# Optimization experiments

Measured on AMD Instinct MI355X. Metric: run time of the kernel, lower is better.

The kernel has to match this reference:

```python
import jax, jax.numpy as jnp
import numpy as np

NUM_CLASSES = 172
IGNORE_INDEX = 255
DICE_WEIGHT = 0.5
EPS = 1e-7


def setup_inputs() -> dict:
    key = jax.random.key(0)
    k1, k2 = jax.random.split(key)
    pred = jax.random.normal(k1, (4, NUM_CLASSES, 256, 256), dtype=jnp.float32)
    target = jax.random.randint(k2, (4, 256, 256), 0, NUM_CLASSES, dtype=jnp.int32)
    return {"pred": pred, "target": target}


def reference(pred, target):
    # pred: [B, C, H, W] logits; target: [B, H, W] int labels (255 = ignore)
    C = NUM_CLASSES
    logp = jax.nn.log_softmax(pred, axis=1)  # [B, C, H, W]

    # ---- cross entropy with ignore_index (mean over valid pixels) ----
    valid = target != IGNORE_INDEX  # [B, H, W]
    safe_tgt = jnp.where(valid, target, 0)
    nll = -jnp.take_along_axis(logp, safe_tgt[:, None].astype(jnp.int32), axis=1)[:, 0]  # [B, H, W]
    n_valid = jnp.sum(valid)
    ce = jnp.sum(jnp.where(valid, nll, 0.0)) / jnp.maximum(n_valid, 1).astype(pred.dtype)

    # ---- dice loss: vectorized over classes (replaces per-class python loop) ----
    p = jnp.exp(logp)  # softmax probs [B, C, H, W]
    # intersection[c] = sum over pixels with target==c of p[:, c] at those pixels
    gathered = jnp.take_along_axis(p, safe_tgt[:, None].astype(jnp.int32), axis=1)[:, 0]  # [B, H, W]
    seg_ids = target.ravel().astype(jnp.int32)  # ignore pixels land in bucket 255, discarded
    inter = jax.ops.segment_sum(gathered.ravel(), seg_ids, num_segments=256)[:C]  # [C]
    counts = jax.ops.segment_sum(jnp.ones_like(gathered.ravel()), seg_ids, num_segments=256)[:C]
    union = jnp.sum(p, axis=(0, 2, 3)) + counts  # [C]
    valid_c = union > 0
    dice_terms = jnp.where(valid_c, (2.0 * inter + EPS) / (union + EPS), 0.0)
    n_valid_c = jnp.sum(valid_c).astype(pred.dtype)
    dice = jnp.where(n_valid_c > 0, 1.0 - jnp.sum(dice_terms) / jnp.maximum(n_valid_c, 1.0), 0.0)

    return ce + DICE_WEIGHT * dice
```

## Files before the change

kernel.cpp:

```cpp
#include <hip/hip_runtime.h>
#include <stdint.h>

#define NCLS 172
#define IGN 255
#define HW 65536
#define NPIX 262144
#define EPSV 1e-7f
#define TP 32
#define TROWS 176
#define NTILE 4
#define PIXPERBLK (TP * NTILE)
#define NSTAGE 32
#define SS 520

__device__ __forceinline__ void gl_lds16(const float* g, float* l) {
    __builtin_amdgcn_global_load_lds(
        (const __attribute__((address_space(1))) void*)g,
        (__attribute__((address_space(3))) void*)l, 16, 0, 0);
}

__global__ __launch_bounds__(256) void seg_fused(
    const float* __restrict__ pred, const int* __restrict__ tgt,
    float* __restrict__ part)
{
    __shared__ float tile[TROWS * TP];
    __shared__ float sPart[128];
    __shared__ float sInvs[TP];
    __shared__ float sInter[NCLS];
    __shared__ unsigned int sCnt[NCLS];

    const int tid   = threadIdx.x;
    const int lane  = tid & 63;
    const int wv    = tid >> 6;
    const int p     = tid & 31;
    const int chunk = tid >> 5;

    for (int i = tid; i < NCLS; i += 256) { sInter[i] = 0.f; sCnt[i] = 0u; }

    const int pix0 = blockIdx.x * PIXPERBLK;
    const int b    = pix0 >> 16;
    const int hw0  = pix0 & (HW - 1);
    const float* gb = pred + (size_t)b * NCLS * HW + hw0;

    const int scb = lane >> 3;
    const int spo = (lane & 7) << 2;

    float unionAcc = 0.f;
    float ceAcc = 0.f, nvAcc = 0.f;

    for (int tI = 0; tI < NTILE; ++tI) {
        const float* gt = gb + tI * TP;

        for (int ib = wv; ib < 22; ib += 4) {
            int cb = ib * 8 + scb;
            if (cb > NCLS - 1) cb = NCLS - 1;
            gl_lds16(gt + (size_t)cb * HW + spo, &tile[ib * (8 * TP)]);
        }
        __syncthreads();

        float s0 = 0.f, s1 = 0.f;
        #pragma unroll
        for (int k = 0; k < 20; k += 2) {
            const int i0 = (chunk + 8 * k) * TP + p;
            const int i1 = (chunk + 8 * k + 8) * TP + p;
            const float e0 = __expf(tile[i0]);
            const float e1 = __expf(tile[i1]);
            tile[i0] = e0; tile[i1] = e1;
            s0 += e0; s1 += e1;
        }
        {   const int i0 = (chunk + 160) * TP + p;
            const float e = __expf(tile[i0]); tile[i0] = e; s0 += e; }
        if (chunk < 4) {
            const int i1 = (chunk + 168) * TP + p;
            const float e = __expf(tile[i1]); tile[i1] = e; s1 += e;
        }
        float sv = s0 + s1;
        sv += __shfl_down(sv, 32, 64);
        if (lane < 32) sPart[wv * 32 + p] = sv;
        __syncthreads();

        if (tid < 32) {
            const float s    = (sPart[p] + sPart[32 + p]) + (sPart[64 + p] + sPart[96 + p]);
            const float invs = 1.0f / s;
            sInvs[p] = invs;
            const int  t     = tgt[pix0 + tI * TP + p];
            const bool valid = (t != IGN);
            const int  st    = valid ? t : 0;
            const float et   = tile[st * TP + p];
            const float pt   = et * invs;
            float nll = valid ? -__logf(pt) : 0.f;
            float nv  = valid ? 1.f : 0.f;
            if (valid) { atomicAdd(&sInter[st], pt); atomicAdd(&sCnt[st], 1u); }
            #pragma unroll
            for (int off = 16; off > 0; off >>= 1) {
                nll += __shfl_down(nll, off, 64);
                nv  += __shfl_down(nv,  off, 64);
            }
            if (tid == 0) { ceAcc += nll; nvAcc += nv; }
        }
        __syncthreads();

        if (tid < NCLS) {
            const float* tr = &tile[tid * TP];
            float u0 = 0.f, u1 = 0.f;
            #pragma unroll
            for (int k = 0; k < TP; k += 2) {
                const int p0 = (tid + k)     & (TP - 1);
                const int p1 = (tid + k + 1) & (TP - 1);
                u0 += tr[p0] * sInvs[p0];
                u1 += tr[p1] * sInvs[p1];
            }
            unionAcc += u0 + u1;
        }
        __syncthreads();
    }

    float* pb = part + (size_t)(blockIdx.x & (NSTAGE - 1)) * SS;
    for (int i = tid; i < NCLS; i += 256) {
        const float vi = sInter[i];
        if (vi != 0.f) atomicAdd(&pb[i], vi);
        const unsigned int ci = sCnt[i];
        if (ci != 0u) atomicAdd(&pb[NCLS + i], (float)ci);
    }
    if (tid < NCLS) atomicAdd(&pb[344 + tid], unionAcc);
    if (tid == 0) { atomicAdd(&pb[516], ceAcc); atomicAdd(&pb[517], nvAcc); }
}

__global__ __launch_bounds__(256) void seg_fin(
    const float* __restrict__ part, float* __restrict__ out)
{
    __shared__ float sT[256], sN[256];
    const int tid = threadIdx.x;
    float term = 0.f, nv = 0.f;
    if (tid < NCLS) {
        float inter = 0.f, cnt = 0.f, uni = 0.f;
        for (int st = 0; st < NSTAGE; ++st) {
            inter += part[st * SS + tid];
            cnt   += part[st * SS + NCLS + tid];
            uni   += part[st * SS + 344 + tid];
        }
        const float u = uni + cnt;
        if (u > 0.f) { term = (2.f * inter + EPSV) / (u + EPSV); nv = 1.f; }
    }
    sT[tid] = term; sN[tid] = nv;
    __syncthreads();
    #pragma unroll
    for (int s2 = 128; s2 > 0; s2 >>= 1) {
        if (tid < s2) { sT[tid] += sT[tid + s2]; sN[tid] += sN[tid + s2]; }
        __syncthreads();
    }
    if (tid == 0) {
        float ce = 0.f, nvl = 0.f;
        for (int st = 0; st < NSTAGE; ++st) {
            ce  += part[st * SS + 516];
            nvl += part[st * SS + 517];
        }
        const float ceo  = ce / fmaxf(nvl, 1.f);
        const float dice = (sN[0] > 0.f) ? (1.f - sT[0] / fmaxf(sN[0], 1.f)) : 0.f;
        out[0] = ceo + 0.5f * dice;
    }
}

extern "C" void kernel_launch(void* const* d_in, const int* in_sizes, int n_in,
                              void* d_out, int out_size, void* d_ws, size_t ws_size,
                              hipStream_t stream) {
    const float* pred = (const float*)d_in[0];
    const int*   tgt  = (const int*)d_in[1];
    float* out  = (float*)d_out;
    float* part = (float*)d_ws;

    hipMemsetAsync(d_ws, 0, NSTAGE * SS * sizeof(float), stream);
    seg_fused<<<NPIX / PIXPERBLK, 256, 0, stream>>>(pred, tgt, part);
    seg_fin<<<1, 256, 0, stream>>>(part, out);
}
```

Baseline: 255.3 us.

## Double-buffer LDS tiles to prefetch next pixel tile during compute

Doubles the LDS tile buffer and issues asynchronous global-to-LDS loads for the next 32-pixel tile before computing the current one, using explicit vmcnt waits and raw barriers instead of __syncthreads. Targets are preloaded into shared memory once per block. This aims to hide global load latency behind the exp/sum and union work. In exchange, LDS use roughly doubles, which may lower occupancy, and the hand-written waitcnt logic is fragile.

```diff
diff --git a/kernel.cpp b/kernel.cpp
--- a/kernel.cpp
+++ b/kernel.cpp
@@ -7,7 +7,8 @@
 #define NPIX 262144
 #define EPSV 1e-7f
 #define TP 32
-#define TROWS 176
+#define TROWS 192
+#define TSZ (TROWS * TP)
 #define NTILE 4
 #define PIXPERBLK (TP * NTILE)
 #define NSTAGE 32
@@ -23,9 +24,10 @@
     const float* __restrict__ pred, const int* __restrict__ tgt,
     float* __restrict__ part)
 {
-    __shared__ float tile[TROWS * TP];
+    __shared__ float tile[2 * TSZ];
     __shared__ float sPart[128];
     __shared__ float sInvs[TP];
+    __shared__ int   sTgt[PIXPERBLK];
     __shared__ float sInter[NCLS];
     __shared__ unsigned int sCnt[NCLS];
 
@@ -36,57 +38,75 @@
     const int chunk = tid >> 5;
 
     for (int i = tid; i < NCLS; i += 256) { sInter[i] = 0.f; sCnt[i] = 0u; }
+    const int pix0 = blockIdx.x * PIXPERBLK;
+    if (tid < PIXPERBLK) sTgt[tid] = tgt[pix0 + tid];
 
-    const int pix0 = blockIdx.x * PIXPERBLK;
-    const int b    = pix0 >> 16;
-    const int hw0  = pix0 & (HW - 1);
+    const int b   = pix0 >> 16;
+    const int hw0 = pix0 & (HW - 1);
     const float* gb = pred + (size_t)b * NCLS * HW + hw0;
 
     const int scb = lane >> 3;
     const int spo = (lane & 7) << 2;
 
-    float unionAcc = 0.f;
-    float ceAcc = 0.f, nvAcc = 0.f;
+    #pragma unroll
+    for (int k = 0; k < 6; ++k) {
+        const int ib = wv + 4 * k;
+        int cb = ib * 8 + scb; if (cb > NCLS - 1) cb = NCLS - 1;
+        gl_lds16(gb + (size_t)cb * HW + spo, &tile[ib * (8 * TP)]);
+    }
+
+    float unionAcc = 0.f, ceAcc = 0.f, nvAcc = 0.f;
 
     for (int tI = 0; tI < NTILE; ++tI) {
-        const float* gt = gb + tI * TP;
+        const int tb = (tI & 1) * TSZ;
 
-        for (int ib = wv; ib < 22; ib += 4) {
-            int cb = ib * 8 + scb;
-            if (cb > NCLS - 1) cb = NCLS - 1;
-            gl_lds16(gt + (size_t)cb * HW + spo, &tile[ib * (8 * TP)]);
+        if (tI + 1 < NTILE) {
+            const float* gt = gb + (tI + 1) * TP;
+            const int nb = ((tI + 1) & 1) * TSZ;
+            #pragma unroll
+            for (int k = 0; k < 6; ++k) {
+                const int ib = wv + 4 * k;
+                int cb = ib * 8 + scb; if (cb > NCLS - 1) cb = NCLS - 1;
+                gl_lds16(gt + (size_t)cb * HW + spo, &tile[nb + ib * (8 * TP)]);
+            }
+            asm volatile("s_waitcnt vmcnt(6) lgkmcnt(0)" ::: "memory");
+        } else {
+            asm volatile("s_waitcnt vmcnt(0) lgkmcnt(0)" ::: "memory");
         }
-        __syncthreads();
+        __builtin_amdgcn_s_barrier();
+        __builtin_amdgcn_sched_barrier(0);
 
         float s0 = 0.f, s1 = 0.f;
         #pragma unroll
         for (int k = 0; k < 20; k += 2) {
-            const int i0 = (chunk + 8 * k) * TP + p;
-            const int i1 = (chunk + 8 * k + 8) * TP + p;
+            const int i0 = tb + (chunk + 8 * k) * TP + p;
+            const int i1 = tb + (chunk + 8 * k + 8) * TP + p;
             const float e0 = __expf(tile[i0]);
             const float e1 = __expf(tile[i1]);
             tile[i0] = e0; tile[i1] = e1;
             s0 += e0; s1 += e1;
         }
-        {   const int i0 = (chunk + 160) * TP + p;
+        {   const int i0 = tb + (chunk + 160) * TP + p;
             const float e = __expf(tile[i0]); tile[i0] = e; s0 += e; }
         if (chunk < 4) {
-            const int i1 = (chunk + 168) * TP + p;
+            const int i1 = tb + (chunk + 168) * TP + p;
             const float e = __expf(tile[i1]); tile[i1] = e; s1 += e;
         }
         float sv = s0 + s1;
         sv += __shfl_down(sv, 32, 64);
         if (lane < 32) sPart[wv * 32 + p] = sv;
-        __syncthreads();
+        asm volatile("s_waitcnt lgkmcnt(0)" ::: "memory");
+        __builtin_amdgcn_s_barrier();
+        __builtin_amdgcn_sched_barrier(0);
 
         if (tid < 32) {
             const float s    = (sPart[p] + sPart[32 + p]) + (sPart[64 + p] + sPart[96 + p]);
             const float invs = 1.0f / s;
             sInvs[p] = invs;
-            const int  t     = tgt[pix0 + tI * TP + p];
+            const int  t     = sTgt[tI * TP + p];
             const bool valid = (t != IGN);
             const int  st    = valid ? t : 0;
-            const float et   = tile[st * TP + p];
+            const float et   = tile[tb + st * TP + p];
             const float pt   = et * invs;
             float nll = valid ? -__logf(pt) : 0.f;
             float nv  = valid ? 1.f : 0.f;
@@ -98,21 +118,25 @@
             }
             if (tid == 0) { ceAcc += nll; nvAcc += nv; }
         }
-        __syncthreads();
+        asm volatile("s_waitcnt lgkmcnt(0)" ::: "memory");
+        __builtin_amdgcn_s_barrier();
+        __builtin_amdgcn_sched_barrier(0);
 
         if (tid < NCLS) {
-            const float* tr = &tile[tid * TP];
+            const int tr = tb + tid * TP;
             float u0 = 0.f, u1 = 0.f;
             #pragma unroll
             for (int k = 0; k < TP; k += 2) {
                 const int p0 = (tid + k)     & (TP - 1);
                 const int p1 = (tid + k + 1) & (TP - 1);
-                u0 += tr[p0] * sInvs[p0];
-                u1 += tr[p1] * sInvs[p1];
+                u0 += tile[tr + p0] * sInvs[p0];
+                u1 += tile[tr + p1] * sInvs[p1];
             }
             unionAcc += u0 + u1;
         }
-        __syncthreads();
+        asm volatile("s_waitcnt lgkmcnt(0)" ::: "memory");
+        __builtin_amdgcn_s_barrier();
+        __builtin_amdgcn_sched_barrier(0);
     }
 
     float* pb = part + (size_t)(blockIdx.x & (NSTAGE - 1)) * SS;
```

New measurement: 256.9 us. No clear change (+0.6%).

## Restructure fused loss kernel: 128-pixel blocks, register-held exps, two-half class staging

Applied to the files above, without the earlier changes.

Each block now handles 128 contiguous pixels with 512 threads instead of 4 sequential 32-pixel tiles. The 172 classes are staged into LDS in two halves, and the exponentials are kept in 43 registers per thread instead of being written back to LDS. The union accumulation moves from a single-threaded-per-class LDS loop to wave shuffle reductions with shared atomics, and target gathering selects the value from registers. This aims to cut LDS footprint and serial phases and give more parallelism per block, at the cost of higher register pressure and many more shuffle reductions and LDS atomics per block.

```diff
diff --git a/kernel.cpp b/kernel.cpp
--- a/kernel.cpp
+++ b/kernel.cpp
@@ -6,10 +6,11 @@
 #define HW 65536
 #define NPIX 262144
 #define EPSV 1e-7f
-#define TP 32
-#define TROWS 176
-#define NTILE 4
-#define PIXPERBLK (TP * NTILE)
+#define TP 128
+#define NTHR 512
+#define HCLS 86
+#define HROWS 96
+#define HSZ (HROWS * TP)
 #define NSTAGE 32
 #define SS 520
 
@@ -19,111 +20,111 @@
         (__attribute__((address_space(3))) void*)l, 16, 0, 0);
 }
 
-__global__ __launch_bounds__(256) void seg_fused(
+__global__ __launch_bounds__(NTHR, 4) void seg_fused(
     const float* __restrict__ pred, const int* __restrict__ tgt,
     float* __restrict__ part)
 {
-    __shared__ float tile[TROWS * TP];
-    __shared__ float sPart[128];
-    __shared__ float sInvs[TP];
+    __shared__ float tile[HSZ];
+    __shared__ float sPart[4 * TP];
+    __shared__ int   sTgt[TP];
     __shared__ float sInter[NCLS];
+    __shared__ float sUnion[NCLS];
     __shared__ unsigned int sCnt[NCLS];
+    __shared__ float sCE[2];
 
     const int tid   = threadIdx.x;
     const int lane  = tid & 63;
     const int wv    = tid >> 6;
-    const int p     = tid & 31;
-    const int chunk = tid >> 5;
+    const int p     = tid & (TP - 1);
+    const int chunk = tid >> 7;
 
-    for (int i = tid; i < NCLS; i += 256) { sInter[i] = 0.f; sCnt[i] = 0u; }
+    for (int i = tid; i < NCLS; i += NTHR) { sInter[i] = 0.f; sUnion[i] = 0.f; sCnt[i] = 0u; }
+    if (tid < 2) sCE[tid] = 0.f;
+    const int pix0 = blockIdx.x * TP;
+    if (tid < TP) sTgt[tid] = tgt[pix0 + tid];
 
-    const int pix0 = blockIdx.x * PIXPERBLK;
-    const int b    = pix0 >> 16;
-    const int hw0  = pix0 & (HW - 1);
+    const int b   = pix0 >> 16;
+    const int hw0 = pix0 & (HW - 1);
     const float* gb = pred + (size_t)b * NCLS * HW + hw0;
 
-    const int scb = lane >> 3;
-    const int spo = (lane & 7) << 2;
+    const int srow = lane >> 5;
+    const int spo  = (lane & 31) << 2;
 
-    float unionAcc = 0.f;
-    float ceAcc = 0.f, nvAcc = 0.f;
+    auto stage = [&](int half) {
+        const int coff = half * HCLS;
+        #pragma unroll
+        for (int k6 = 0; k6 < 6; ++k6) {
+            const int ib = wv + 8 * k6;
+            int c = coff + 2 * ib + srow;
+            if (c > NCLS - 1) c = NCLS - 1;
+            gl_lds16(gb + (size_t)c * HW + spo, &tile[ib * 256]);
+        }
+    };
 
-    for (int tI = 0; tI < NTILE; ++tI) {
-        const float* gt = gb + tI * TP;
+    float e[43];
+    float sAcc = 0.f;
 
-        for (int ib = wv; ib < 22; ib += 4) {
-            int cb = ib * 8 + scb;
-            if (cb > NCLS - 1) cb = NCLS - 1;
-            gl_lds16(gt + (size_t)cb * HW + spo, &tile[ib * (8 * TP)]);
-        }
-        __syncthreads();
+    stage(0);
+    __syncthreads();
+    #pragma unroll
+    for (int k = 0; k < 43; ++k) {
+        const int c = chunk + 4 * k;
+        if (c < HCLS) { e[k] = __expf(tile[c * TP + p]); sAcc += e[k]; }
+        else          { e[k] = 0.f; }
+    }
+    __syncthreads();
 
-        float s0 = 0.f, s1 = 0.f;
+    stage(1);
+    __syncthreads();
+    #pragma unroll
+    for (int k = 0; k < 43; ++k) {
+        const int c = chunk + 4 * k;
+        if (c >= HCLS) { e[k] = __expf(tile[(c - HCLS) * TP + p]); sAcc += e[k]; }
+    }
+    sPart[chunk * TP + p] = sAcc;
+    __syncthreads();
+
+    const float s = (sPart[p] + sPart[TP + p]) + (sPart[2 * TP + p] + sPart[3 * TP + p]);
+    const float invs = 1.0f / s;
+
+    const int t = sTgt[p];
+    const bool valid = (t != IGN);
+    float nll = 0.f, nv = 0.f;
+    if (valid && (t & 3) == chunk) {
+        float pt = 0.f;
         #pragma unroll
-        for (int k = 0; k < 20; k += 2) {
-            const int i0 = (chunk + 8 * k) * TP + p;
-            const int i1 = (chunk + 8 * k + 8) * TP + p;
-            const float e0 = __expf(tile[i0]);
-            const float e1 = __expf(tile[i1]);
-            tile[i0] = e0; tile[i1] = e1;
-            s0 += e0; s1 += e1;
-        }
-        {   const int i0 = (chunk + 160) * TP + p;
-            const float e = __expf(tile[i0]); tile[i0] = e; s0 += e; }
-        if (chunk < 4) {
-            const int i1 = (chunk + 168) * TP + p;
-            const float e = __expf(tile[i1]); tile[i1] = e; s1 += e;
-        }
-        float sv = s0 + s1;
-        sv += __shfl_down(sv, 32, 64);
-        if (lane < 32) sPart[wv * 32 + p] = sv;
-        __syncthreads();
+        for (int k = 0; k < 43; ++k)
+            if ((t >> 2) == k) pt = e[k];
+        pt *= invs;
+        nll = -__logf(pt); nv = 1.f;
+        atomicAdd(&sInter[t], pt);
+        atomicAdd(&sCnt[t], 1u);
+    }
+    #pragma unroll
+    for (int off = 32; off > 0; off >>= 1) {
+        nll += __shfl_down(nll, off, 64);
+        nv  += __shfl_down(nv,  off, 64);
+    }
+    if (lane == 0 && nv != 0.f) { atomicAdd(&sCE[0], nll); atomicAdd(&sCE[1], nv); }
 
-        if (tid < 32) {
-            const float s    = (sPart[p] + sPart[32 + p]) + (sPart[64 + p] + sPart[96 + p]);
-            const float invs = 1.0f / s;
-            sInvs[p] = invs;
-            const int  t     = tgt[pix0 + tI * TP + p];
-            const bool valid = (t != IGN);
-            const int  st    = valid ? t : 0;
-            const float et   = tile[st * TP + p];
-            const float pt   = et * invs;
-            float nll = valid ? -__logf(pt) : 0.f;
-            float nv  = valid ? 1.f : 0.f;
-            if (valid) { atomicAdd(&sInter[st], pt); atomicAdd(&sCnt[st], 1u); }
-            #pragma unroll
-            for (int off = 16; off > 0; off >>= 1) {
-                nll += __shfl_down(nll, off, 64);
-                nv  += __shfl_down(nv,  off, 64);
-            }
-            if (tid == 0) { ceAcc += nll; nvAcc += nv; }
-        }
-        __syncthreads();
-
-        if (tid < NCLS) {
-            const float* tr = &tile[tid * TP];
-            float u0 = 0.f, u1 = 0.f;
-            #pragma unroll
-            for (int k = 0; k < TP; k += 2) {
-                const int p0 = (tid + k)     & (TP - 1);
-                const int p1 = (tid + k + 1) & (TP - 1);
-                u0 += tr[p0] * sInvs[p0];
-                u1 += tr[p1] * sInvs[p1];
-            }
-            unionAcc += u0 + u1;
-        }
-        __syncthreads();
+    #pragma unroll
+    for (int k = 0; k < 43; ++k) {
+        float v = e[k] * invs;
+        #pragma unroll
+        for (int m = 32; m > 0; m >>= 1) v += __shfl_xor(v, m, 64);
+        if (lane == 0) atomicAdd(&sUnion[chunk + 4 * k], v);
     }
+    __syncthreads();
 
     float* pb = part + (size_t)(blockIdx.x & (NSTAGE - 1)) * SS;
-    for (int i = tid; i < NCLS; i += 256) {
-        const float vi = sInter[i];
-        if (vi != 0.f) atomicAdd(&pb[i], vi);
-        const unsigned int ci = sCnt[i];
-        if (ci != 0u) atomicAdd(&pb[NCLS + i], (float)ci);
+    if (tid < NCLS) {
+        const float vi = sInter[tid];
+        if (vi != 0.f) atomicAdd(&pb[tid], vi);
+        const unsigned int ci = sCnt[tid];
+        if (ci != 0u) atomicAdd(&pb[NCLS + tid], (float)ci);
+        atomicAdd(&pb[344 + tid], sUnion[tid]);
     }
-    if (tid < NCLS) atomicAdd(&pb[344 + tid], unionAcc);
-    if (tid == 0) { atomicAdd(&pb[516], ceAcc); atomicAdd(&pb[517], nvAcc); }
+    if (tid == 0) { atomicAdd(&pb[516], sCE[0]); atomicAdd(&pb[517], sCE[1]); }
 }
 
 __global__ __launch_bounds__(256) void seg_fin(
@@ -170,6 +171,6 @@
     float* part = (float*)d_ws;
 
     hipMemsetAsync(d_ws, 0, NSTAGE * SS * sizeof(float), stream);
-    seg_fused<<<NPIX / PIXPERBLK, 256, 0, stream>>>(pred, tgt, part);
+    seg_fused<<<NPIX / TP, NTHR, 0, stream>>>(pred, tgt, part);
     seg_fin<<<1, 256, 0, stream>>>(part, out);
 }
```

Result: slower. 282.0 us (+10.5%).
